# Kernel tuning notes

Hardware: AMD Instinct MI355X
Metric: run time of the kernel (lower is better)

The kernel has to match this reference:

```python
import jax, jax.numpy as jnp
import numpy as np

NUM_LEVELS = 4
RADIUS = 4


def _bilinear_zeros(img, x, y):
    # img: (N, Hl, Wl); x, y: (N, K) pixel coords (align_corners=True identity map).
    # Replicates F.grid_sample(mode='bilinear', padding_mode='zeros', align_corners=True).
    N, Hl, Wl = img.shape
    x0 = jnp.floor(x); y0 = jnp.floor(y)
    wx1 = x - x0; wx0 = 1.0 - wx1
    wy1 = y - y0; wy0 = 1.0 - wy1
    bidx = jnp.arange(N)[:, None]

    def gather(xi, yi):
        inb = (xi >= 0) & (xi <= Wl - 1) & (yi >= 0) & (yi <= Hl - 1)
        xc = jnp.clip(xi, 0, Wl - 1).astype(jnp.int32)
        yc = jnp.clip(yi, 0, Hl - 1).astype(jnp.int32)
        vals = img[bidx, yc, xc]
        return jnp.where(inb, vals, jnp.zeros((), img.dtype))

    return (wy0 * wx0 * gather(x0, y0) + wy0 * wx1 * gather(x0 + 1, y0)
            + wy1 * wx0 * gather(x0, y0 + 1) + wy1 * wx1 * gather(x0 + 1, y0 + 1))


def setup_inputs() -> dict:
    key = jax.random.key(0)
    k1, k2, k3 = jax.random.split(key, 3)
    B, C, H, W = 2, 256, 64, 64
    fmap1 = jax.random.normal(k1, (B, C, H, W), dtype=jnp.float32)
    fmap2 = jax.random.normal(k2, (B, C, H, W), dtype=jnp.float32)
    # coords = base pixel grid + small random flow (stays mostly in-bounds)
    ys, xs = jnp.meshgrid(jnp.arange(H, dtype=jnp.float32), jnp.arange(W, dtype=jnp.float32), indexing='ij')
    grid = jnp.stack([xs, ys], axis=0)[None]  # (1, 2, H, W), channel0 = x
    flow = (jax.random.uniform(k3, (B, 2, H, W), dtype=jnp.float32) - 0.5) * 20.0
    coords = grid + flow
    return {'fmap1': fmap1, 'fmap2': fmap2, 'coords': coords}


def reference(fmap1, fmap2, coords):
    B, C, H, W = fmap1.shape
    HW = H * W
    # all-pairs correlation: (B, HW, HW), scaled by 1/sqrt(C)
    corr = jnp.einsum('bci,bcj->bij', fmap1.reshape(B, C, HW), fmap2.reshape(B, C, HW))
    corr = corr / jnp.sqrt(jnp.asarray(C, fmap1.dtype))
    corr = corr.reshape(B * HW, H, W)
    pyramid = [corr]
    for _ in range(NUM_LEVELS - 1):
        N, Hl, Wl = corr.shape
        corr = corr.reshape(N, Hl // 2, 2, Wl // 2, 2).mean(axis=(2, 4))  # avg_pool2d(2,2)
        pyramid.append(corr)

    r = RADIUS
    dy = jnp.linspace(-r, r, 2 * r + 1, dtype=coords.dtype)
    dx = jnp.linspace(-r, r, 2 * r + 1, dtype=coords.dtype)
    gy, gx = jnp.meshgrid(dy, dx, indexing='ij')  # matches torch.meshgrid(dy, dx)
    d0 = gy.reshape(-1); d1 = gx.reshape(-1)      # K = (2r+1)^2

    cperm = coords.transpose(0, 2, 3, 1).reshape(B * HW, 2)  # (N, 2), [:,0]=x, [:,1]=y
    outs = []
    for i, corr_l in enumerate(pyramid):
        cl = cperm / (2.0 ** i)
        # coords_lvl = centroid + delta; xgrid uses delta[...,0]=dy grid, ygrid uses delta[...,1]=dx grid
        x = cl[:, 0:1] + d0[None, :]
        y = cl[:, 1:2] + d1[None, :]
        outs.append(_bilinear_zeros(corr_l, x, y))  # (N, K)
    out = jnp.concatenate(outs, axis=-1)            # (N, num_levels*K)
    out = out.reshape(B, H, W, -1).transpose(0, 3, 1, 2)  # (B, 324, H, W)
    return out
```

## Files before the change

kernel.cpp:

```cpp
#include <hip/hip_runtime.h>
#include <cstdint>

#define B2 2
#define CCH 256
#define HH 64
#define WW 64
#define HWHW 4096
#define KOUT 324

typedef _Float16 half_t;
typedef _Float16 h2 __attribute__((ext_vector_type(2)));

__device__ __forceinline__ float fdot2f(h2 a, h2 b, float c) {
#if __has_builtin(__builtin_amdgcn_fdot2)
  return __builtin_amdgcn_fdot2(a, b, c, false);
#else
  return c + (float)a.x * (float)b.x + (float)a.y * (float)b.y;
#endif
}

__global__ __launch_bounds__(256) void transpose_cl(
    const float* __restrict__ f1, const float* __restrict__ f2,
    half_t* __restrict__ f1t, half_t* __restrict__ f2t) {
  __shared__ float tile[32][33];
  int zz = blockIdx.z;
  const float* src = (zz < 2) ? f1 : f2;
  half_t* dst = (zz < 2) ? f1t : f2t;
  float s = (zz < 2) ? 0.0625f : 1.0f;
  int b = zz & 1;
  int hw0 = blockIdx.x * 32;
  int c0 = blockIdx.y * 32;
  int tx = threadIdx.x;
  int ty = threadIdx.y;
  const float* sb = src + (size_t)b * CCH * HWHW;
  half_t* db = dst + (size_t)b * HWHW * CCH;
#pragma unroll
  for (int i = 0; i < 4; i++)
    tile[ty + i * 8][tx] = sb[(size_t)(c0 + ty + i * 8) * HWHW + hw0 + tx];
  __syncthreads();
#pragma unroll
  for (int i = 0; i < 4; i++)
    db[(size_t)(hw0 + ty + i * 8) * CCH + c0 + tx] = (half_t)(tile[tx][ty + i * 8] * s);
}

__global__ __launch_bounds__(256) void pool_all(
    const h2* __restrict__ l0, h2* __restrict__ l1,
    h2* __restrict__ l2, h2* __restrict__ l3) {
  int idx = blockIdx.x * blockDim.x + threadIdx.x;
  const int n1 = B2 * 32 * 32 * 128;
  const int n2 = B2 * 16 * 16 * 128;
  const int n3 = B2 * 8 * 8 * 128;
  int L, Wo, local;
  h2* dst;
  if (idx < n1) { L = 1; Wo = 32; local = idx; dst = l1; }
  else if (idx < n1 + n2) { L = 2; Wo = 16; local = idx - n1; dst = l2; }
  else if (idx < n1 + n2 + n3) { L = 3; Wo = 8; local = idx - n1 - n2; dst = l3; }
  else return;
  int f = 1 << L;
  int sh = 6 - L;
  int c2 = local & 127;
  int t = local >> 7;
  int x = t & (Wo - 1);
  int y = (t >> sh) & (Wo - 1);
  int b = t >> (2 * sh);
  const h2* src = l0 + (size_t)b * HWHW * 128 + c2;
  float ax = 0.f, ay = 0.f;
  for (int dy = 0; dy < f; dy++)
    for (int dx = 0; dx < f; dx++) {
      h2 a = src[(size_t)((y * f + dy) * WW + (x * f + dx)) * 128];
      ax += (float)a.x; ay += (float)a.y;
    }
  float s = 1.0f / (float)(f * f);
  h2 r;
  r.x = (half_t)(ax * s);
  r.y = (half_t)(ay * s);
  dst[local] = r;
}

__device__ __forceinline__ float dpp_sum16(float x) {
  int v;
  v = __builtin_amdgcn_update_dpp(0, __float_as_int(x), 0xB1, 0xF, 0xF, true);
  x += __int_as_float(v);
  v = __builtin_amdgcn_update_dpp(0, __float_as_int(x), 0x4E, 0xF, 0xF, true);
  x += __int_as_float(v);
  v = __builtin_amdgcn_update_dpp(0, __float_as_int(x), 0x141, 0xF, 0xF, true);
  x += __int_as_float(v);
  v = __builtin_amdgcn_update_dpp(0, __float_as_int(x), 0x140, 0xF, 0xF, true);
  x += __int_as_float(v);
  return x;
}

__global__ __launch_bounds__(512, 4) void sample16(
    const float* __restrict__ coords,
    const half_t* __restrict__ f1t,
    const half_t* __restrict__ f2l0, const half_t* __restrict__ f2l1,
    const half_t* __restrict__ f2l2, const half_t* __restrict__ f2l3,
    float* __restrict__ out) {
  __shared__ float4 f1s4[512];
  __shared__ float4 l3img[2048];
  __shared__ float P[4][16][100];
  __shared__ float wgt[4][16][4];
  __shared__ float cxy[2][16];

  int bid = blockIdx.x;
  int g = ((bid & 7) << 6) | (bid >> 3);
  int n0 = g << 4;
  int b = n0 >> 12;
  int i0 = n0 & 4095;
  int yi = i0 >> 6;
  int x0 = i0 & 63;
  int tid = threadIdx.x;

  f1s4[tid] = ((const float4*)(f1t + (size_t)n0 * CCH))[tid];
  {
    const float4* l3g = (const float4*)(f2l3 + (size_t)b * 64 * CCH);
#pragma unroll
    for (int r = 0; r < 4; r++) l3img[tid + r * 512] = l3g[tid + r * 512];
  }
  if (tid < 32) {
    int q = tid & 15, c = tid >> 4;
    cxy[c][q] = coords[(size_t)(b * 2 + c) * HWHW + i0 + q];
  }
  __syncthreads();

  int w = tid >> 6;
  int l = w >> 1;
  int h = w & 1;
  int lane = tid & 63;
  int lg = lane >> 4;
  int l16 = lane & 15;

  float inv = 1.0f / (float)(1 << l);
  int Hl = HH >> l, Wl = WW >> l;
  const half_t* f2 = (l == 0) ? f2l0 : (l == 1) ? f2l1 : f2l2;
  const float4* f2b = (const float4*)(f2) + (size_t)b * Hl * Wl * 32 + l16;
  const float4* l3b = l3img + l16;
  const h2* f1h = (const h2*)f1s4;

  for (int qq = 0; qq < 8; qq++) {
    int q = h * 8 + qq;
    float clx = cxy[0][q], cly = cxy[1][q];
    float xl = clx * inv, yl = cly * inv;
    float fx = floorf(xl), fy = floorf(yl);
    int ix0 = (int)fx - 4, iy0 = (int)fy - 4;
    float wx1 = xl - fx, wy1 = yl - fy;
    if (lane == 0) {
      wgt[l][q][0] = 1.0f - wx1; wgt[l][q][1] = wx1;
      wgt[l][q][2] = 1.0f - wy1; wgt[l][q][3] = wy1;
    }
    int fi = q * 128 + l16 * 4;
    h2 fa0 = f1h[fi + 0], fa1 = f1h[fi + 1], fa2 = f1h[fi + 2], fa3 = f1h[fi + 3];
    h2 fb0 = f1h[fi + 64], fb1 = f1h[fi + 65], fb2 = f1h[fi + 66], fb3 = f1h[fi + 67];

    int u = 0, v = lg, t = lg;
    if (l == 3) {
      for (int it = 0; it < 25; it++) {
        int txp = ix0 + u, typ = iy0 + v;
        bool inb = ((unsigned)txp < (unsigned)Wl) & ((unsigned)typ < (unsigned)Hl);
        float d = 0.0f;
        if (inb) {
          const float4* tp = l3b + (size_t)(typ * 8 + txp) * 32;
          float4 A = tp[0];
          float4 Bv = tp[16];
          const h2* ah = (const h2*)&A;
          const h2* bh = (const h2*)&Bv;
          d = fdot2f(ah[0], fa0, d); d = fdot2f(ah[1], fa1, d);
          d = fdot2f(ah[2], fa2, d); d = fdot2f(ah[3], fa3, d);
          d = fdot2f(bh[0], fb0, d); d = fdot2f(bh[1], fb1, d);
          d = fdot2f(bh[2], fb2, d); d = fdot2f(bh[3], fb3, d);
        }
        d = dpp_sum16(d);
        if (l16 == 0) P[l][q][t] = d;
        t += 4; v += 4;
        bool wrap = v >= 10;
        v = wrap ? v - 10 : v;
        u = wrap ? u + 1 : u;
      }
    } else {
      for (int it = 0; it < 25; it++) {
        int txp = ix0 + u, typ = iy0 + v;
        bool inb = ((unsigned)txp < (unsigned)Wl) & ((unsigned)typ < (unsigned)Hl);
        float d = 0.0f;
        if (inb) {
          const float4* tp = f2b + (size_t)(typ * Wl + txp) * 32;
          float4 A = tp[0];
          float4 Bv = tp[16];
          const h2* ah = (const h2*)&A;
          const h2* bh = (const h2*)&Bv;
          d = fdot2f(ah[0], fa0, d); d = fdot2f(ah[1], fa1, d);
          d = fdot2f(ah[2], fa2, d); d = fdot2f(ah[3], fa3, d);
          d = fdot2f(bh[0], fb0, d); d = fdot2f(bh[1], fb1, d);
          d = fdot2f(bh[2], fb2, d); d = fdot2f(bh[3], fb3, d);
        }
        d = dpp_sum16(d);
        if (l16 == 0) P[l][q][t] = d;
        t += 4; v += 4;
        bool wrap = v >= 10;
        v = wrap ? v - 10 : v;
        u = wrap ? u + 1 : u;
      }
    }
  }
  __syncthreads();

  int limit = h ? 40 : 41;
#pragma unroll
  for (int kk = 0; kk < 11; kk++) {
    int idx = kk * 64 + lane;
    int kl = idx >> 4;
    int q = idx & 15;
    if (kl < limit) {
      int k = h * 41 + kl;
      int a = k / 9, bb2 = k - a * 9;
      float wx0 = wgt[l][q][0], wx1 = wgt[l][q][1];
      float wy0 = wgt[l][q][2], wy1 = wgt[l][q][3];
      const float* Pq = P[l][q];
      float val = wy0 * (wx0 * Pq[a * 10 + bb2] + wx1 * Pq[(a + 1) * 10 + bb2])
                + wy1 * (wx0 * Pq[a * 10 + bb2 + 1] + wx1 * Pq[(a + 1) * 10 + bb2 + 1]);
      out[(size_t)(b * KOUT + l * 81 + k) * HWHW + (size_t)yi * WW + x0 + q] = val;
    }
  }
}

extern "C" void kernel_launch(void* const* d_in, const int* in_sizes, int n_in,
                              void* d_out, int out_size, void* d_ws, size_t ws_size,
                              hipStream_t stream) {
  const float* fmap1 = (const float*)d_in[0];
  const float* fmap2 = (const float*)d_in[1];
  const float* coords = (const float*)d_in[2];
  float* out = (float*)d_out;

  char* ws = (char*)d_ws;
  half_t* f1t  = (half_t*)(ws);
  half_t* f2l0 = (half_t*)(ws + ((size_t)4 << 20));
  half_t* f2l1 = (half_t*)(ws + ((size_t)8 << 20));
  half_t* f2l2 = (half_t*)(ws + ((size_t)9 << 20));
  half_t* f2l3 = (half_t*)(ws + ((size_t)9 << 20) + ((size_t)512 << 10));

  dim3 tb(32, 8, 1);
  dim3 tg(HWHW / 32, CCH / 32, 4);
  transpose_cl<<<tg, tb, 0, stream>>>(fmap1, fmap2, f1t, f2l0);

  int npool = B2 * (32 * 32 + 16 * 16 + 8 * 8) * 128;
  pool_all<<<(npool + 255) / 256, 256, 0, stream>>>(
      (const h2*)f2l0, (h2*)f2l1, (h2*)f2l2, (h2*)f2l3);

  sample16<<<512, 512, 0, stream>>>(coords, f1t, f2l0, f2l1, f2l2, f2l3, out);
}
```

Before: 154.7 us.

## Compute full level-2/3 correlation with MFMA and sample from it

```diff
diff --git a/kernel.cpp b/kernel.cpp
--- a/kernel.cpp
+++ b/kernel.cpp
@@ -10,6 +10,8 @@
 
 typedef _Float16 half_t;
 typedef _Float16 h2 __attribute__((ext_vector_type(2)));
+typedef _Float16 h8 __attribute__((ext_vector_type(8)));
+typedef float f32x4 __attribute__((ext_vector_type(4)));
 
 __device__ __forceinline__ float fdot2f(h2 a, h2 b, float c) {
 #if __has_builtin(__builtin_amdgcn_fdot2)
@@ -77,6 +79,41 @@
   dst[local] = r;
 }
 
+__global__ __launch_bounds__(256) void corr23_k(
+    const half_t* __restrict__ f1t,
+    const half_t* __restrict__ f2l2, const half_t* __restrict__ f2l3,
+    float* __restrict__ corr) {
+  int bid = blockIdx.x;
+  int g = ((bid & 7) << 6) | (bid >> 3);
+  int n0 = g << 4;
+  int b = n0 >> 12;
+  int w = threadIdx.x >> 6;
+  int l = threadIdx.x & 63;
+  int row = l & 15;
+  int kg = l >> 4;
+
+  const h8* A = (const h8*)(f1t + ((size_t)(n0 + row) * CCH) + kg * 8);
+  h8 a[8];
+#pragma unroll
+  for (int ks = 0; ks < 8; ks++) a[ks] = A[ks * 4];
+
+  for (int nt = w * 5; nt < w * 5 + 5; nt++) {
+    const half_t* Bb = (nt < 16)
+        ? f2l2 + ((size_t)b * 256 + nt * 16) * CCH
+        : f2l3 + ((size_t)b * 64 + (nt - 16) * 16) * CCH;
+    const h8* Bp = (const h8*)(Bb + (size_t)row * CCH + kg * 8);
+    f32x4 acc = {0.f, 0.f, 0.f, 0.f};
+#pragma unroll
+    for (int ks = 0; ks < 8; ks++)
+      acc = __builtin_amdgcn_mfma_f32_16x16x32_f16(a[ks], Bp[ks * 4], acc, 0, 0, 0);
+#pragma unroll
+    for (int r = 0; r < 4; r++) {
+      int q = kg * 4 + r;
+      corr[(size_t)(n0 + q) * 320 + nt * 16 + row] = acc[r];
+    }
+  }
+}
+
 __device__ __forceinline__ float dpp_sum16(float x) {
   int v;
   v = __builtin_amdgcn_update_dpp(0, __float_as_int(x), 0xB1, 0xF, 0xF, true);
@@ -90,16 +127,15 @@
   return x;
 }
 
-__global__ __launch_bounds__(512, 4) void sample16(
+__global__ __launch_bounds__(512, 4) void sample16b(
     const float* __restrict__ coords,
     const half_t* __restrict__ f1t,
     const half_t* __restrict__ f2l0, const half_t* __restrict__ f2l1,
-    const half_t* __restrict__ f2l2, const half_t* __restrict__ f2l3,
+    const float* __restrict__ corr,
     float* __restrict__ out) {
   __shared__ float4 f1s4[512];
-  __shared__ float4 l3img[2048];
-  __shared__ float P[4][16][100];
-  __shared__ float wgt[4][16][4];
+  __shared__ float P[2][16][100];
+  __shared__ float wgt[2][16][4];
   __shared__ float cxy[2][16];
 
   int bid = blockIdx.x;
@@ -112,11 +148,6 @@
   int tid = threadIdx.x;
 
   f1s4[tid] = ((const float4*)(f1t + (size_t)n0 * CCH))[tid];
-  {
-    const float4* l3g = (const float4*)(f2l3 + (size_t)b * 64 * CCH);
-#pragma unroll
-    for (int r = 0; r < 4; r++) l3img[tid + r * 512] = l3g[tid + r * 512];
-  }
   if (tid < 32) {
     int q = tid & 15, c = tid >> 4;
     cxy[c][q] = coords[(size_t)(b * 2 + c) * HWHW + i0 + q];
@@ -124,21 +155,19 @@
   __syncthreads();
 
   int w = tid >> 6;
-  int l = w >> 1;
-  int h = w & 1;
+  int l = w >> 2;
   int lane = tid & 63;
   int lg = lane >> 4;
   int l16 = lane & 15;
 
-  float inv = 1.0f / (float)(1 << l);
+  float inv = (l == 0) ? 1.0f : 0.5f;
   int Hl = HH >> l, Wl = WW >> l;
-  const half_t* f2 = (l == 0) ? f2l0 : (l == 1) ? f2l1 : f2l2;
+  const half_t* f2 = (l == 0) ? f2l0 : f2l1;
   const float4* f2b = (const float4*)(f2) + (size_t)b * Hl * Wl * 32 + l16;
-  const float4* l3b = l3img + l16;
   const h2* f1h = (const h2*)f1s4;
 
-  for (int qq = 0; qq < 8; qq++) {
-    int q = h * 8 + qq;
+  for (int qq = 0; qq < 4; qq++) {
+    int q = (w & 3) * 4 + qq;
     float clx = cxy[0][q], cly = cxy[1][q];
     float xl = clx * inv, yl = cly * inv;
     float fx = floorf(xl), fy = floorf(yl);
@@ -153,71 +182,84 @@
     h2 fb0 = f1h[fi + 64], fb1 = f1h[fi + 65], fb2 = f1h[fi + 66], fb3 = f1h[fi + 67];
 
     int u = 0, v = lg, t = lg;
-    if (l == 3) {
-      for (int it = 0; it < 25; it++) {
-        int txp = ix0 + u, typ = iy0 + v;
-        bool inb = ((unsigned)txp < (unsigned)Wl) & ((unsigned)typ < (unsigned)Hl);
-        float d = 0.0f;
-        if (inb) {
-          const float4* tp = l3b + (size_t)(typ * 8 + txp) * 32;
-          float4 A = tp[0];
-          float4 Bv = tp[16];
-          const h2* ah = (const h2*)&A;
-          const h2* bh = (const h2*)&Bv;
-          d = fdot2f(ah[0], fa0, d); d = fdot2f(ah[1], fa1, d);
-          d = fdot2f(ah[2], fa2, d); d = fdot2f(ah[3], fa3, d);
-          d = fdot2f(bh[0], fb0, d); d = fdot2f(bh[1], fb1, d);
-          d = fdot2f(bh[2], fb2, d); d = fdot2f(bh[3], fb3, d);
-        }
-        d = dpp_sum16(d);
-        if (l16 == 0) P[l][q][t] = d;
-        t += 4; v += 4;
-        bool wrap = v >= 10;
-        v = wrap ? v - 10 : v;
-        u = wrap ? u + 1 : u;
-      }
-    } else {
-      for (int it = 0; it < 25; it++) {
-        int txp = ix0 + u, typ = iy0 + v;
-        bool inb = ((unsigned)txp < (unsigned)Wl) & ((unsigned)typ < (unsigned)Hl);
-        float d = 0.0f;
-        if (inb) {
-          const float4* tp = f2b + (size_t)(typ * Wl + txp) * 32;
-          float4 A = tp[0];
-          float4 Bv = tp[16];
-          const h2* ah = (const h2*)&A;
-          const h2* bh = (const h2*)&Bv;
-          d = fdot2f(ah[0], fa0, d); d = fdot2f(ah[1], fa1, d);
-          d = fdot2f(ah[2], fa2, d); d = fdot2f(ah[3], fa3, d);
-          d = fdot2f(bh[0], fb0, d); d = fdot2f(bh[1], fb1, d);
-          d = fdot2f(bh[2], fb2, d); d = fdot2f(bh[3], fb3, d);
-        }
-        d = dpp_sum16(d);
-        if (l16 == 0) P[l][q][t] = d;
-        t += 4; v += 4;
-        bool wrap = v >= 10;
-        v = wrap ? v - 10 : v;
-        u = wrap ? u + 1 : u;
-      }
+    for (int it = 0; it < 25; it++) {
+      int txp = ix0 + u, typ = iy0 + v;
+      bool inb = ((unsigned)txp < (unsigned)Wl) & ((unsigned)typ < (unsigned)Hl);
+      float d = 0.0f;
+      if (inb) {
+        const float4* tp = f2b + (size_t)(typ * Wl + txp) * 32;
+        float4 A = tp[0];
+        float4 Bv = tp[16];
+        const h2* ah = (const h2*)&A;
+        const h2* bh = (const h2*)&Bv;
+        d = fdot2f(ah[0], fa0, d); d = fdot2f(ah[1], fa1, d);
+        d = fdot2f(ah[2], fa2, d); d = fdot2f(ah[3], fa3, d);
+        d = fdot2f(bh[0], fb0, d); d = fdot2f(bh[1], fb1, d);
+        d = fdot2f(bh[2], fb2, d); d = fdot2f(bh[3], fb3, d);
+      }
+      d = dpp_sum16(d);
+      if (l16 == 0) P[l][q][t] = d;
+      t += 4; v += 4;
+      bool wrap = v >= 10;
+      v = wrap ? v - 10 : v;
+      u = wrap ? u + 1 : u;
     }
   }
   __syncthreads();
 
-  int limit = h ? 40 : 41;
-#pragma unroll
-  for (int kk = 0; kk < 11; kk++) {
-    int idx = kk * 64 + lane;
-    int kl = idx >> 4;
-    int q = idx & 15;
-    if (kl < limit) {
-      int k = h * 41 + kl;
+#pragma unroll
+  for (int it = 0; it < 6; it++) {
+    int kidx = it * 32 + (tid >> 4);
+    if (kidx < 162) {
+      int lvl = kidx >= 81;
+      int k = kidx - 81 * lvl;
+      int q = tid & 15;
       int a = k / 9, bb2 = k - a * 9;
-      float wx0 = wgt[l][q][0], wx1 = wgt[l][q][1];
-      float wy0 = wgt[l][q][2], wy1 = wgt[l][q][3];
-      const float* Pq = P[l][q];
+      float wx0 = wgt[lvl][q][0], wx1 = wgt[lvl][q][1];
+      float wy0 = wgt[lvl][q][2], wy1 = wgt[lvl][q][3];
+      const float* Pq = P[lvl][q];
       float val = wy0 * (wx0 * Pq[a * 10 + bb2] + wx1 * Pq[(a + 1) * 10 + bb2])
                 + wy1 * (wx0 * Pq[a * 10 + bb2 + 1] + wx1 * Pq[(a + 1) * 10 + bb2 + 1]);
-      out[(size_t)(b * KOUT + l * 81 + k) * HWHW + (size_t)yi * WW + x0 + q] = val;
+      out[(size_t)(b * KOUT + lvl * 81 + k) * HWHW + (size_t)yi * WW + x0 + q] = val;
+    }
+  }
+
+#pragma unroll
+  for (int it = 0; it < 6; it++) {
+    int kidx = it * 32 + (tid >> 4);
+    if (kidx < 162) {
+      int lvl = 2 + (kidx >= 81);
+      int k = kidx - 81 * (kidx >= 81);
+      int q = tid & 15;
+      float inv2 = (lvl == 2) ? 0.25f : 0.125f;
+      int Wl2 = (lvl == 2) ? 16 : 8;
+      int base = (lvl == 2) ? 0 : 256;
+      float xl = cxy[0][q] * inv2, yl = cxy[1][q] * inv2;
+      float fx = floorf(xl), fy = floorf(yl);
+      int ix0 = (int)fx - 4, iy0 = (int)fy - 4;
+      float wx1 = xl - fx, wx0 = 1.0f - wx1;
+      float wy1 = yl - fy, wy0 = 1.0f - wy1;
+      const float* cq = corr + (size_t)(n0 + q) * 320 + base;
+      int a = k / 9, bb2 = k - a * 9;
+      float p00 = 0.f, p10 = 0.f, p01 = 0.f, p11 = 0.f;
+      {
+        int x = ix0 + a, y = iy0 + bb2;
+        if (((unsigned)x < (unsigned)Wl2) & ((unsigned)y < (unsigned)Wl2)) p00 = cq[y * Wl2 + x];
+      }
+      {
+        int x = ix0 + a + 1, y = iy0 + bb2;
+        if (((unsigned)x < (unsigned)Wl2) & ((unsigned)y < (unsigned)Wl2)) p10 = cq[y * Wl2 + x];
+      }
+      {
+        int x = ix0 + a, y = iy0 + bb2 + 1;
+        if (((unsigned)x < (unsigned)Wl2) & ((unsigned)y < (unsigned)Wl2)) p01 = cq[y * Wl2 + x];
+      }
+      {
+        int x = ix0 + a + 1, y = iy0 + bb2 + 1;
+        if (((unsigned)x < (unsigned)Wl2) & ((unsigned)y < (unsigned)Wl2)) p11 = cq[y * Wl2 + x];
+      }
+      float val = wy0 * (wx0 * p00 + wx1 * p10) + wy1 * (wx0 * p01 + wx1 * p11);
+      out[(size_t)(b * KOUT + lvl * 81 + k) * HWHW + (size_t)yi * WW + x0 + q] = val;
     }
   }
 }
@@ -236,6 +278,7 @@
   half_t* f2l1 = (half_t*)(ws + ((size_t)8 << 20));
   half_t* f2l2 = (half_t*)(ws + ((size_t)9 << 20));
   half_t* f2l3 = (half_t*)(ws + ((size_t)9 << 20) + ((size_t)512 << 10));
+  float*  corr = (float*)(ws + ((size_t)10 << 20));
 
   dim3 tb(32, 8, 1);
   dim3 tg(HWHW / 32, CCH / 32, 4);
@@ -245,5 +288,7 @@
   pool_all<<<(npool + 255) / 256, 256, 0, stream>>>(
       (const h2*)f2l0, (h2*)f2l1, (h2*)f2l2, (h2*)f2l3);
 
-  sample16<<<512, 512, 0, stream>>>(coords, f1t, f2l0, f2l1, f2l2, f2l3, out);
-}
+  corr23_k<<<512, 256, 0, stream>>>(f1t, f2l2, f2l3, corr);
+
+  sample16b<<<512, 512, 0, stream>>>(coords, f1t, f2l0, f2l1, corr, out);
+}
```

Result: faster. 147.8 us (-4.4%).
